# Optimization experiments

Hardware: AMD Instinct MI355X
Metric: run time of the kernel (lower is better)

The kernel has to match this reference:

```python
import jax, jax.numpy as jnp
import numpy as np

DIM = 1024
HEADS = 16
DH = DIM // HEADS
RANK = 4
B, S = 4, 1024
SCALE = 1.0 / np.sqrt(DH)
LN_EPS = 1e-5


def layer_norm(x, g, b):
    mu = jnp.mean(x, axis=-1, keepdims=True)
    var = jnp.mean((x - mu) ** 2, axis=-1, keepdims=True)
    return (x - mu) * jax.lax.rsqrt(var + LN_EPS) * g + b


def setup_inputs() -> dict:
    key = jax.random.key(0)
    ks = jax.random.split(key, 12)
    xav = lambda k, o, i: jax.random.uniform(k, (o, i), jnp.float32, -1.0, 1.0) * np.sqrt(6.0 / (o + i))
    return {
        "x": jax.random.normal(ks[0], (B, S, DIM), jnp.float32),
        "sigma": jnp.float32(0.1),
        "U": jax.random.normal(ks[1], (DIM, RANK), jnp.float32),
        "V": jax.random.normal(ks[2], (RANK, DIM), jnp.float32),
        "W_proj1": xav(ks[3], DIM, DIM // 2),
        "b_proj1": jnp.zeros((DIM,), jnp.float32),
        "W_proj2": xav(ks[4], DIM, DIM // 2),
        "b_proj2": jnp.zeros((DIM,), jnp.float32),
        "W_qkv1": xav(ks[5], 3 * DIM, DIM),
        "W_qkv2": xav(ks[6], 3 * DIM, DIM),
        "W_out": xav(ks[7], DIM, DIM),
        "b_out": jnp.zeros((DIM,), jnp.float32),
        "ln_g": jnp.ones((DIM,), jnp.float32),
        "ln_b": jnp.zeros((DIM,), jnp.float32),
    }


def _heads(t):  # [B,S,D] -> [B,H,S,dh]
    return t.reshape(B, S, HEADS, DH).transpose(0, 2, 1, 3)


def reference(x, sigma, U, V, W_proj1, b_proj1, W_proj2, b_proj2,
              W_qkv1, W_qkv2, W_out, b_out, ln_g, ln_b):
    # SVD adaptation bias: sigma*(U@V) summed over last dim -> [D], broadcast add
    svd_adapt = jnp.sum(sigma * (U @ V), axis=-1)  # [D]
    adapted_x = x + svd_adapt  # broadcast over [B,S,D]

    x1, x2 = jnp.split(adapted_x, 2, axis=-1)  # each [B,S,D/2]
    x1 = x1 @ W_proj1.T + b_proj1  # [B,S,D]
    x2 = x2 @ W_proj2.T + b_proj2

    q1, k1, v1 = jnp.split(x1 @ W_qkv1.T, 3, axis=-1)
    q2, k2, v2 = jnp.split(x2 @ W_qkv2.T, 3, axis=-1)
    q1, k1, v1 = _heads(q1), _heads(k1), _heads(v1)
    q2, k2, v2 = _heads(q2), _heads(k2), _heads(v2)

    # differential attention: softmax(q1k1) - softmax(q2k2), applied to (v1+v2)/2
    attn1 = jax.nn.softmax(jnp.einsum("bhqd,bhkd->bhqk", q1, k1) * SCALE, axis=-1)
    attn2 = jax.nn.softmax(jnp.einsum("bhqd,bhkd->bhqk", q2, k2) * SCALE, axis=-1)
    diff = attn1 - attn2
    out = jnp.einsum("bhqk,bhkd->bhqd", diff, (v1 + v2) * 0.5)

    out = out.transpose(0, 2, 1, 3).reshape(B, S, DIM)
    out = out @ W_out.T + b_out
    return layer_norm(out, ln_g, ln_b)
```

## Files before the change

### kernel.cpp

```cpp
#include <hip/hip_runtime.h>
#include <hip/hip_bf16.h>
#include <math.h>

#define DIMN   1024
#define HEADS  16
#define DHEAD  64
#define BQKV   3072
#define BATCH  4
#define SEQ    1024
#define NROWS  (BATCH * SEQ)
#define ATT_SCALE 0.125f
#define LN_EPS 1e-5f

typedef __attribute__((ext_vector_type(8))) short  bf16x8;
typedef __attribute__((ext_vector_type(4))) float  f32x4;
typedef __attribute__((ext_vector_type(4))) unsigned short u16x4;

__device__ __forceinline__ unsigned short f2bf(float f) {
    unsigned u = __float_as_uint(f);
    u += 0x7FFFu + ((u >> 16) & 1u);
    return (unsigned short)(u >> 16);
}
__device__ __forceinline__ float bf2f(unsigned short h) {
    return __uint_as_float((unsigned)h << 16);
}
__device__ __forceinline__ void gload_lds16(const void* g, void* l) {
    __builtin_amdgcn_global_load_lds(
        (const __attribute__((address_space(1))) unsigned int*)g,
        (__attribute__((address_space(3))) unsigned int*)l, 16, 0, 0);
}

__global__ __launch_bounds__(1024) void svd_kernel(
    const float* __restrict__ U, const float* __restrict__ V,
    const float* __restrict__ sigma_p, float* __restrict__ svd)
{
    __shared__ float part[16][4];
    __shared__ float vsum[4];
    const int tid = threadIdx.x;
    float v0 = V[0 * DIMN + tid];
    float v1 = V[1 * DIMN + tid];
    float v2 = V[2 * DIMN + tid];
    float v3 = V[3 * DIMN + tid];
    #pragma unroll
    for (int off = 32; off > 0; off >>= 1) {
        v0 += __shfl_down(v0, off);
        v1 += __shfl_down(v1, off);
        v2 += __shfl_down(v2, off);
        v3 += __shfl_down(v3, off);
    }
    const int lane = tid & 63, w = tid >> 6;
    if (lane == 0) { part[w][0] = v0; part[w][1] = v1; part[w][2] = v2; part[w][3] = v3; }
    __syncthreads();
    if (tid < 4) {
        float s = 0.f;
        #pragma unroll
        for (int i = 0; i < 16; ++i) s += part[i][tid];
        vsum[tid] = s;
    }
    __syncthreads();
    const float sg = sigma_p[0];
    float acc = U[tid * 4 + 0] * vsum[0] + U[tid * 4 + 1] * vsum[1]
              + U[tid * 4 + 2] * vsum[2] + U[tid * 4 + 3] * vsum[3];
    svd[tid] = sg * acc;
}

__global__ __launch_bounds__(256) void cvt_kernel(
    const float* __restrict__ src, unsigned short* __restrict__ dst)
{
    const int i = (blockIdx.x * 256 + threadIdx.x) * 8;
    float4 a = *(const float4*)(src + i);
    float4 b = *(const float4*)(src + i + 4);
    u16x4 h0, h1;
    h0[0] = f2bf(a.x); h0[1] = f2bf(a.y); h0[2] = f2bf(a.z); h0[3] = f2bf(a.w);
    h1[0] = f2bf(b.x); h1[1] = f2bf(b.y); h1[2] = f2bf(b.z); h1[3] = f2bf(b.w);
    *(u16x4*)(dst + i) = h0;
    *(u16x4*)(dst + i + 4) = h1;
}

__global__ __launch_bounds__(256) void xadapt_kernel(
    const float* __restrict__ x, const float* __restrict__ svd,
    unsigned short* __restrict__ out)
{
    const int i = (blockIdx.x * 256 + threadIdx.x) * 8;
    const int d = i & (DIMN - 1);
    float4 a = *(const float4*)(x + i);
    float4 b = *(const float4*)(x + i + 4);
    float4 sa = *(const float4*)(svd + d);
    float4 sb = *(const float4*)(svd + d + 4);
    u16x4 h0, h1;
    h0[0] = f2bf(a.x + sa.x); h0[1] = f2bf(a.y + sa.y);
    h0[2] = f2bf(a.z + sa.z); h0[3] = f2bf(a.w + sa.w);
    h1[0] = f2bf(b.x + sb.x); h1[1] = f2bf(b.y + sb.y);
    h1[2] = f2bf(b.z + sb.z); h1[3] = f2bf(b.w + sb.w);
    *(u16x4*)(out + i) = h0;
    *(u16x4*)(out + i + 4) = h1;
}

#define GBM 128
#define GBN 128
#define GBK 64

__global__ __launch_bounds__(256, 2) void gemm_bf16(
    const unsigned short* __restrict__ A, int lda,
    const unsigned short* __restrict__ W, int ldw,
    const float* __restrict__ bias,
    void* __restrict__ C, int ldc, int K, int out_bf16)
{
    __shared__ __align__(16) short As[GBM * GBK];
    __shared__ __align__(16) short Bs[GBN * GBK];
    const int tid = threadIdx.x;
    const int m0 = blockIdx.y * GBM;
    const int n0 = blockIdx.x * GBN;
    const int lane = tid & 63;
    const int wv = tid >> 6;
    const int wr = wv >> 1, wc = wv & 1;
    const int lr = lane & 15;
    const int kg = lane >> 4;

    f32x4 acc[4][4];
    #pragma unroll
    for (int i = 0; i < 4; ++i)
        #pragma unroll
        for (int j = 0; j < 4; ++j)
            acc[i][j] = (f32x4){0.f, 0.f, 0.f, 0.f};

    for (int k0 = 0; k0 < K; k0 += GBK) {
        #pragma unroll
        for (int i = 0; i < 4; ++i) {
            int flat = i * 256 + tid;
            int r = flat >> 3, c = flat & 7;
            int sc = c ^ (r & 7);
            gload_lds16(A + (size_t)(m0 + r) * lda + k0 + sc * 8, As + flat * 8);
        }
        #pragma unroll
        for (int i = 0; i < 4; ++i) {
            int flat = i * 256 + tid;
            int r = flat >> 3, c = flat & 7;
            int sc = c ^ (r & 7);
            gload_lds16(W + (size_t)(n0 + r) * ldw + k0 + sc * 8, Bs + flat * 8);
        }
        __syncthreads();

        #pragma unroll
        for (int ks = 0; ks < 2; ++ks) {
            bf16x8 a[4], b[4];
            #pragma unroll
            for (int mi = 0; mi < 4; ++mi) {
                int row = wr * 64 + mi * 16 + lr;
                int boff = row * 128 + (((ks * 4 + kg) ^ (row & 7)) << 4);
                a[mi] = *(const bf16x8*)((const char*)As + boff);
            }
            #pragma unroll
            for (int ni = 0; ni < 4; ++ni) {
                int row = wc * 64 + ni * 16 + lr;
                int boff = row * 128 + (((ks * 4 + kg) ^ (row & 7)) << 4);
                b[ni] = *(const bf16x8*)((const char*)Bs + boff);
            }
            #pragma unroll
            for (int mi = 0; mi < 4; ++mi)
                #pragma unroll
                for (int ni = 0; ni < 4; ++ni)
                    acc[mi][ni] = __builtin_amdgcn_mfma_f32_16x16x32_bf16(
                        a[mi], b[ni], acc[mi][ni], 0, 0, 0);
        }
        __syncthreads();
    }

    #pragma unroll
    for (int ni = 0; ni < 4; ++ni) {
        const int col = n0 + wc * 64 + ni * 16 + lr;
        const float bs = bias ? bias[col] : 0.f;
        #pragma unroll
        for (int mi = 0; mi < 4; ++mi) {
            const int row = m0 + wr * 64 + mi * 16 + kg * 4;
            #pragma unroll
            for (int r = 0; r < 4; ++r) {
                float v = acc[mi][ni][r] + bs;
                if (out_bf16)
                    ((unsigned short*)C)[(size_t)(row + r) * ldc + col] = f2bf(v);
                else
                    ((float*)C)[(size_t)(row + r) * ldc + col] = v;
            }
        }
    }
}

__global__ __launch_bounds__(256, 2) void attn_mfma(
    const unsigned short* __restrict__ qkv1,
    const unsigned short* __restrict__ qkv2,
    unsigned short* __restrict__ out)
{
    __shared__ __align__(16) short k1s[64 * 64];
    __shared__ __align__(16) short k2s[64 * 64];
    __shared__ __align__(16) short vts[64 * 64];
    __shared__ __align__(16) short pbufs[4][16 * 64];

    const int tid = threadIdx.x;
    const int lane = tid & 63;
    const int wv = tid >> 6;
    const int lr = lane & 15;
    const int kg = lane >> 4;
    const int bh = blockIdx.y;
    const int b = bh >> 4, h = bh & 15;
    const int bS = b * SEQ;
    const int q0w = blockIdx.x * 64 + wv * 16;
    short* pw = pbufs[wv];

    bf16x8 qf1[2], qf2[2];
    {
        const size_t qrow = (size_t)(bS + q0w + lr) * BQKV + h * DHEAD;
        #pragma unroll
        for (int ks = 0; ks < 2; ++ks) {
            const unsigned short* p1 = qkv1 + qrow + ks * 32 + kg * 8;
            const unsigned short* p2 = qkv2 + qrow + ks * 32 + kg * 8;
            bf16x8 f;
            #pragma unroll
            for (int j = 0; j < 8; ++j) f[j] = (short)f2bf(bf2f(p1[j]) * ATT_SCALE);
            qf1[ks] = f;
            #pragma unroll
            for (int j = 0; j < 8; ++j) f[j] = (short)f2bf(bf2f(p2[j]) * ATT_SCALE);
            qf2[ks] = f;
        }
    }

    f32x4 o1[4], o2[4];
    #pragma unroll
    for (int i = 0; i < 4; ++i) {
        o1[i] = (f32x4){0.f, 0.f, 0.f, 0.f};
        o2[i] = (f32x4){0.f, 0.f, 0.f, 0.f};
    }
    float m1 = -1e30f, l1 = 0.f, m2 = -1e30f, l2 = 0.f;

    for (int kt = 0; kt < SEQ; kt += 64) {
        #pragma unroll
        for (int i = 0; i < 2; ++i) {
            int flat = i * 256 + tid;
            int r = flat >> 3, c = flat & 7;
            int sc = c ^ (r & 7);
            size_t g = (size_t)(bS + kt + r) * BQKV + 1024 + h * DHEAD + sc * 8;
            gload_lds16(qkv1 + g, k1s + flat * 8);
            gload_lds16(qkv2 + g, k2s + flat * 8);
        }
        #pragma unroll
        for (int i = 0; i < 2; ++i) {
            int idx = i * 256 + tid;
            int kp = idx & 31;
            int dg = idx >> 5;
            size_t g = (size_t)(bS + kt + 2 * kp) * BQKV + 2048 + h * DHEAD + dg * 4;
            u16x4 x0 = *(const u16x4*)(qkv1 + g);
            u16x4 y0 = *(const u16x4*)(qkv2 + g);
            u16x4 x1 = *(const u16x4*)(qkv1 + g + BQKV);
            u16x4 y1 = *(const u16x4*)(qkv2 + g + BQKV);
            #pragma unroll
            for (int j = 0; j < 4; ++j) {
                float a = 0.5f * (bf2f(x0[j]) + bf2f(y0[j]));
                float c = 0.5f * (bf2f(x1[j]) + bf2f(y1[j]));
                unsigned pk = (unsigned)f2bf(a) | ((unsigned)f2bf(c) << 16);
                int dim = dg * 4 + j;
                int boff = dim * 128 + ((((kp >> 2) ^ (dim & 7)) << 4) | ((kp & 3) << 2));
                *(unsigned*)((char*)vts + boff) = pk;
            }
        }
        __syncthreads();

        f32x4 s1[4], s2[4];
        #pragma unroll
        for (int f = 0; f < 4; ++f) {
            s1[f] = (f32x4){0.f, 0.f, 0.f, 0.f};
            s2[f] = (f32x4){0.f, 0.f, 0.f, 0.f};
        }
        #pragma unroll
        for (int ks = 0; ks < 2; ++ks) {
            #pragma unroll
            for (int f = 0; f < 4; ++f) {
                int row = f * 16 + lr;
                int boff = row * 128 + (((ks * 4 + kg) ^ (row & 7)) << 4);
                bf16x8 a1 = *(const bf16x8*)((const char*)k1s + boff);
                bf16x8 a2 = *(const bf16x8*)((const char*)k2s + boff);
                s1[f] = __builtin_amdgcn_mfma_f32_16x16x32_bf16(a1, qf1[ks], s1[f], 0, 0, 0);
                s2[f] = __builtin_amdgcn_mfma_f32_16x16x32_bf16(a2, qf2[ks], s2[f], 0, 0, 0);
            }
        }

        #pragma unroll
        for (int br = 0; br < 2; ++br) {
            f32x4* sf = br ? s2 : s1;
            float& m = br ? m2 : m1;
            float& l = br ? l2 : l1;
            f32x4* oacc = br ? o2 : o1;

            float tm = -1e30f;
            #pragma unroll
            for (int f = 0; f < 4; ++f)
                #pragma unroll
                for (int r = 0; r < 4; ++r) tm = fmaxf(tm, sf[f][r]);
            tm = fmaxf(tm, __shfl_xor(tm, 16));
            tm = fmaxf(tm, __shfl_xor(tm, 32));
            float mnew = fmaxf(m, tm);
            float sc = __expf(m - mnew);
            m = mnew;

            float psum = 0.f;
            #pragma unroll
            for (int f = 0; f < 4; ++f) {
                u16x4 hw;
                #pragma unroll
                for (int r = 0; r < 4; ++r) {
                    float p = __expf(sf[f][r] - mnew);
                    unsigned short hb = f2bf(p);
                    hw[r] = hb;
                    psum += bf2f(hb);
                }
                int boff = lr * 128 + ((((f * 2 + (kg >> 1)) ^ (lr & 7)) << 4) | ((kg & 1) << 3));
                *(u16x4*)((char*)pw + boff) = hw;
            }
            psum += __shfl_xor(psum, 16);
            psum += __shfl_xor(psum, 32);
            l = l * sc + psum;

            #pragma unroll
            for (int r = 0; r < 4; ++r) {
                float scr = __shfl(sc, (kg << 2) | r);
                #pragma unroll
                for (int nf = 0; nf < 4; ++nf) oacc[nf][r] *= scr;
            }

            #pragma unroll
            for (int ks = 0; ks < 2; ++ks) {
                int boffp = lr * 128 + (((ks * 4 + kg) ^ (lr & 7)) << 4);
                bf16x8 ap = *(const bf16x8*)((const char*)pw + boffp);
                #pragma unroll
                for (int nf = 0; nf < 4; ++nf) {
                    int dim = nf * 16 + lr;
                    int boffv = dim * 128 + (((ks * 4 + kg) ^ (dim & 7)) << 4);
                    bf16x8 bv = *(const bf16x8*)((const char*)vts + boffv);
                    oacc[nf] = __builtin_amdgcn_mfma_f32_16x16x32_bf16(ap, bv, oacc[nf], 0, 0, 0);
                }
            }
        }
        __syncthreads();
    }

    const float inv1 = 1.f / l1, inv2 = 1.f / l2;
    #pragma unroll
    for (int r = 0; r < 4; ++r) {
        float r1 = __shfl(inv1, (kg << 2) | r);
        float r2 = __shfl(inv2, (kg << 2) | r);
        unsigned short* op = out + (size_t)(bS + q0w + kg * 4 + r) * DIMN + h * DHEAD + lr;
        #pragma unroll
        for (int nf = 0; nf < 4; ++nf)
            op[nf * 16] = f2bf(o1[nf][r] * r1 - o2[nf][r] * r2);
    }
}

__global__ __launch_bounds__(256) void ln_kernel(
    const float* __restrict__ X, const float* __restrict__ g,
    const float* __restrict__ bi, float* __restrict__ out)
{
    __shared__ float red[8];
    const int row = blockIdx.x;
    const int tid = threadIdx.x;
    const float* xp = X + (size_t)row * DIMN;
    float4 xv = *(const float4*)(xp + tid * 4);
    float s = xv.x + xv.y + xv.z + xv.w;
    #pragma unroll
    for (int off = 32; off > 0; off >>= 1) s += __shfl_down(s, off);
    const int lane = tid & 63, w = tid >> 6;
    if (lane == 0) red[w] = s;
    __syncthreads();
    const float mu = (red[0] + red[1] + red[2] + red[3]) * (1.f / DIMN);
    const float d0 = xv.x - mu, d1 = xv.y - mu, d2 = xv.z - mu, d3 = xv.w - mu;
    float sq = d0 * d0 + d1 * d1 + d2 * d2 + d3 * d3;
    #pragma unroll
    for (int off = 32; off > 0; off >>= 1) sq += __shfl_down(sq, off);
    if (lane == 0) red[4 + w] = sq;
    __syncthreads();
    const float var = (red[4] + red[5] + red[6] + red[7]) * (1.f / DIMN);
    const float inv = rsqrtf(var + LN_EPS);
    float4 gv = *(const float4*)(g + tid * 4);
    float4 bv = *(const float4*)(bi + tid * 4);
    float4 ov;
    ov.x = d0 * inv * gv.x + bv.x;
    ov.y = d1 * inv * gv.y + bv.y;
    ov.z = d2 * inv * gv.z + bv.z;
    ov.w = d3 * inv * gv.w + bv.w;
    *(float4*)(out + (size_t)row * DIMN + tid * 4) = ov;
}

extern "C" void kernel_launch(void* const* d_in, const int* in_sizes, int n_in,
                              void* d_out, int out_size, void* d_ws, size_t ws_size,
                              hipStream_t stream)
{
    const float* x     = (const float*)d_in[0];
    const float* sigma = (const float*)d_in[1];
    const float* U     = (const float*)d_in[2];
    const float* V     = (const float*)d_in[3];
    const float* Wp1   = (const float*)d_in[4];
    const float* bp1   = (const float*)d_in[5];
    const float* Wp2   = (const float*)d_in[6];
    const float* bp2   = (const float*)d_in[7];
    const float* Wqkv1 = (const float*)d_in[8];
    const float* Wqkv2 = (const float*)d_in[9];
    const float* Wout  = (const float*)d_in[10];
    const float* bout  = (const float*)d_in[11];
    const float* lng   = (const float*)d_in[12];
    const float* lnb   = (const float*)d_in[13];

    const size_t MB = 1024 * 1024;
    char* ws = (char*)d_ws;
    float*          svd    = (float*)(ws);
    unsigned short* wp1b   = (unsigned short*)(ws + 4096);
    unsigned short* wp2b   = (unsigned short*)(ws + 4096 + 1 * MB);
    unsigned short* wq1b   = (unsigned short*)(ws + 4096 + 2 * MB);
    unsigned short* wq2b   = (unsigned short*)(ws + 4096 + 8 * MB);
    unsigned short* woutb  = (unsigned short*)(ws + 4096 + 14 * MB);
    unsigned short* xadapt = (unsigned short*)(ws + 4096 + 16 * MB);
    unsigned short* x1p    = (unsigned short*)(ws + 4096 + 24 * MB);
    unsigned short* x2p    = (unsigned short*)(ws + 4096 + 32 * MB);
    unsigned short* qkv1b  = (unsigned short*)(ws + 4096 + 40 * MB);
    unsigned short* qkv2b  = (unsigned short*)(ws + 4096 + 64 * MB);
    unsigned short* attno  = (unsigned short*)(ws + 4096 + 88 * MB);
    float*          bufO   = (float*)(ws + 4096 + 96 * MB);

    svd_kernel<<<1, 1024, 0, stream>>>(U, V, sigma, svd);

    cvt_kernel<<<256,  256, 0, stream>>>(Wp1,   wp1b);
    cvt_kernel<<<256,  256, 0, stream>>>(Wp2,   wp2b);
    cvt_kernel<<<1536, 256, 0, stream>>>(Wqkv1, wq1b);
    cvt_kernel<<<1536, 256, 0, stream>>>(Wqkv2, wq2b);
    cvt_kernel<<<512,  256, 0, stream>>>(Wout,  woutb);
    xadapt_kernel<<<2048, 256, 0, stream>>>(x, svd, xadapt);

    gemm_bf16<<<dim3(DIMN / GBN, NROWS / GBM), 256, 0, stream>>>(
        xadapt, DIMN, wp1b, DIMN / 2, bp1, x1p, DIMN, DIMN / 2, 1);
    gemm_bf16<<<dim3(DIMN / GBN, NROWS / GBM), 256, 0, stream>>>(
        xadapt + DIMN / 2, DIMN, wp2b, DIMN / 2, bp2, x2p, DIMN, DIMN / 2, 1);
    gemm_bf16<<<dim3(BQKV / GBN, NROWS / GBM), 256, 0, stream>>>(
        x1p, DIMN, wq1b, DIMN, nullptr, qkv1b, BQKV, DIMN, 1);
    gemm_bf16<<<dim3(BQKV / GBN, NROWS / GBM), 256, 0, stream>>>(
        x2p, DIMN, wq2b, DIMN, nullptr, qkv2b, BQKV, DIMN, 1);

    attn_mfma<<<dim3(SEQ / 64, BATCH * HEADS), 256, 0, stream>>>(qkv1b, qkv2b, attno);

    gemm_bf16<<<dim3(DIMN / GBN, NROWS / GBM), 256, 0, stream>>>(
        attno, DIMN, woutb, DIMN, bout, bufO, DIMN, DIMN, 0);

    ln_kernel<<<NROWS, 256, 0, stream>>>(bufO, lng, lnb, (float*)d_out);
}
```

Before: 367.9 us.

## Fold projection weights into QKV weights and prefetch K/V tiles in attention

```diff
diff --git a/kernel.cpp b/kernel.cpp
--- a/kernel.cpp
+++ b/kernel.cpp
@@ -96,9 +96,211 @@
     *(u16x4*)(out + i + 4) = h1;
 }
 
-#define GBM 128
-#define GBN 128
-#define GBK 64
+__global__ __launch_bounds__(256, 2) void wprep_kernel(
+    const float* __restrict__ Wq1, const float* __restrict__ Wp1,
+    const float* __restrict__ Wq2, const float* __restrict__ Wp2,
+    unsigned short* __restrict__ Wt1, unsigned short* __restrict__ Wt2)
+{
+    const float* Wq = blockIdx.z ? Wq2 : Wq1;
+    const float* Wp = blockIdx.z ? Wp2 : Wp1;
+    unsigned short* Wt = blockIdx.z ? Wt2 : Wt1;
+
+    __shared__ __align__(16) short As[128 * 64];
+    __shared__ __align__(16) short Bs[128 * 64];
+    const int tid = threadIdx.x;
+    const int m0 = blockIdx.y * 128;
+    const int n0 = blockIdx.x * 128;
+    const int lane = tid & 63;
+    const int wv = tid >> 6;
+    const int wr = wv >> 1, wc = wv & 1;
+    const int lr = lane & 15;
+    const int kg = lane >> 4;
+
+    f32x4 acc[4][4];
+    #pragma unroll
+    for (int i = 0; i < 4; ++i)
+        #pragma unroll
+        for (int j = 0; j < 4; ++j)
+            acc[i][j] = (f32x4){0.f, 0.f, 0.f, 0.f};
+
+    for (int k0 = 0; k0 < DIMN; k0 += 64) {
+        #pragma unroll
+        for (int i = 0; i < 8; ++i) {
+            int flat = i * 256 + tid;
+            int r  = flat >> 4;
+            int c4 = flat & 15;
+            float4 av = *(const float4*)(Wq + (size_t)(m0 + r) * DIMN + k0 + c4 * 4);
+            u16x4 h;
+            h[0] = f2bf(av.x); h[1] = f2bf(av.y); h[2] = f2bf(av.z); h[3] = f2bf(av.w);
+            int boff = r * 128 + ((((c4 >> 1) ^ (r & 7)) << 4) | ((c4 & 1) << 3));
+            *(u16x4*)((char*)As + boff) = h;
+        }
+        #pragma unroll
+        for (int i = 0; i < 4; ++i) {
+            int idx = i * 256 + tid;
+            int kp = idx & 31;
+            int dg = idx >> 5;
+            const float* p0 = Wp + (size_t)(k0 + 2 * kp) * 512 + n0 + dg * 4;
+            float4 x0 = *(const float4*)p0;
+            float4 x1 = *(const float4*)(p0 + 512);
+            float a0[4] = {x0.x, x0.y, x0.z, x0.w};
+            float a1[4] = {x1.x, x1.y, x1.z, x1.w};
+            #pragma unroll
+            for (int j = 0; j < 4; ++j) {
+                unsigned pk = (unsigned)f2bf(a0[j]) | ((unsigned)f2bf(a1[j]) << 16);
+                int n = dg * 4 + j;
+                int boff = n * 128 + ((((kp >> 2) ^ (n & 7)) << 4) | ((kp & 3) << 2));
+                *(unsigned*)((char*)Bs + boff) = pk;
+            }
+        }
+        __syncthreads();
+
+        #pragma unroll
+        for (int ks = 0; ks < 2; ++ks) {
+            bf16x8 a[4], b[4];
+            #pragma unroll
+            for (int mi = 0; mi < 4; ++mi) {
+                int row = wr * 64 + mi * 16 + lr;
+                int boff = row * 128 + (((ks * 4 + kg) ^ (row & 7)) << 4);
+                a[mi] = *(const bf16x8*)((const char*)As + boff);
+            }
+            #pragma unroll
+            for (int ni = 0; ni < 4; ++ni) {
+                int row = wc * 64 + ni * 16 + lr;
+                int boff = row * 128 + (((ks * 4 + kg) ^ (row & 7)) << 4);
+                b[ni] = *(const bf16x8*)((const char*)Bs + boff);
+            }
+            #pragma unroll
+            for (int mi = 0; mi < 4; ++mi)
+                #pragma unroll
+                for (int ni = 0; ni < 4; ++ni)
+                    acc[mi][ni] = __builtin_amdgcn_mfma_f32_16x16x32_bf16(
+                        a[mi], b[ni], acc[mi][ni], 0, 0, 0);
+        }
+        __syncthreads();
+    }
+
+    #pragma unroll
+    for (int ni = 0; ni < 4; ++ni) {
+        const int col = n0 + wc * 64 + ni * 16 + lr;
+        #pragma unroll
+        for (int mi = 0; mi < 4; ++mi) {
+            const int row = m0 + wr * 64 + mi * 16 + kg * 4;
+            #pragma unroll
+            for (int r = 0; r < 4; ++r) {
+                float sc = (row + r) < DIMN ? ATT_SCALE : 1.f;
+                Wt[(size_t)(row + r) * 512 + col] = f2bf(acc[mi][ni][r] * sc);
+            }
+        }
+    }
+}
+
+__global__ __launch_bounds__(256) void bvec_kernel(
+    const float* __restrict__ Wq1, const float* __restrict__ bp1,
+    const float* __restrict__ Wq2, const float* __restrict__ bp2,
+    float* __restrict__ bt1, float* __restrict__ bt2)
+{
+    const float* Wq = blockIdx.y ? Wq2 : Wq1;
+    const float* bp = blockIdx.y ? bp2 : bp1;
+    float* bt = blockIdx.y ? bt2 : bt1;
+    const int i = blockIdx.x * 256 + threadIdx.x;
+    const float* row = Wq + (size_t)i * DIMN;
+    float s = 0.f;
+    for (int k = 0; k < DIMN; k += 4) {
+        float4 wv = *(const float4*)(row + k);
+        float4 bv = *(const float4*)(bp + k);
+        s += wv.x * bv.x + wv.y * bv.y + wv.z * bv.z + wv.w * bv.w;
+    }
+    bt[i] = (i < DIMN ? ATT_SCALE : 1.f) * s;
+}
+
+__global__ __launch_bounds__(256, 2) void gemm_qkv(
+    const unsigned short* __restrict__ xadapt,
+    const unsigned short* __restrict__ Wt1,
+    const unsigned short* __restrict__ Wt2,
+    const float* __restrict__ bt1,
+    const float* __restrict__ bt2,
+    unsigned short* __restrict__ C1,
+    unsigned short* __restrict__ C2)
+{
+    const unsigned short* A = xadapt + (blockIdx.z ? 512 : 0);
+    const unsigned short* W = blockIdx.z ? Wt2 : Wt1;
+    const float* bias = blockIdx.z ? bt2 : bt1;
+    unsigned short* C = blockIdx.z ? C2 : C1;
+
+    __shared__ __align__(16) short As[128 * 64];
+    __shared__ __align__(16) short Bs[128 * 64];
+    const int tid = threadIdx.x;
+    const int m0 = blockIdx.y * 128;
+    const int n0 = blockIdx.x * 128;
+    const int lane = tid & 63;
+    const int wv = tid >> 6;
+    const int wr = wv >> 1, wc = wv & 1;
+    const int lr = lane & 15;
+    const int kg = lane >> 4;
+
+    f32x4 acc[4][4];
+    #pragma unroll
+    for (int i = 0; i < 4; ++i)
+        #pragma unroll
+        for (int j = 0; j < 4; ++j)
+            acc[i][j] = (f32x4){0.f, 0.f, 0.f, 0.f};
+
+    for (int k0 = 0; k0 < 512; k0 += 64) {
+        #pragma unroll
+        for (int i = 0; i < 4; ++i) {
+            int flat = i * 256 + tid;
+            int r = flat >> 3, c = flat & 7;
+            int sc = c ^ (r & 7);
+            gload_lds16(A + (size_t)(m0 + r) * DIMN + k0 + sc * 8, As + flat * 8);
+        }
+        #pragma unroll
+        for (int i = 0; i < 4; ++i) {
+            int flat = i * 256 + tid;
+            int r = flat >> 3, c = flat & 7;
+            int sc = c ^ (r & 7);
+            gload_lds16(W + (size_t)(n0 + r) * 512 + k0 + sc * 8, Bs + flat * 8);
+        }
+        __syncthreads();
+
+        #pragma unroll
+        for (int ks = 0; ks < 2; ++ks) {
+            bf16x8 a[4], b[4];
+            #pragma unroll
+            for (int mi = 0; mi < 4; ++mi) {
+                int row = wr * 64 + mi * 16 + lr;
+                int boff = row * 128 + (((ks * 4 + kg) ^ (row & 7)) << 4);
+                a[mi] = *(const bf16x8*)((const char*)As + boff);
+            }
+            #pragma unroll
+            for (int ni = 0; ni < 4; ++ni) {
+                int row = wc * 64 + ni * 16 + lr;
+                int boff = row * 128 + (((ks * 4 + kg) ^ (row & 7)) << 4);
+                b[ni] = *(const bf16x8*)((const char*)Bs + boff);
+            }
+            #pragma unroll
+            for (int mi = 0; mi < 4; ++mi)
+                #pragma unroll
+                for (int ni = 0; ni < 4; ++ni)
+                    acc[mi][ni] = __builtin_amdgcn_mfma_f32_16x16x32_bf16(
+                        a[mi], b[ni], acc[mi][ni], 0, 0, 0);
+        }
+        __syncthreads();
+    }
+
+    #pragma unroll
+    for (int ni = 0; ni < 4; ++ni) {
+        const int col = n0 + wc * 64 + ni * 16 + lr;
+        const float bs = bias[col];
+        #pragma unroll
+        for (int mi = 0; mi < 4; ++mi) {
+            const int row = m0 + wr * 64 + mi * 16 + kg * 4;
+            #pragma unroll
+            for (int r = 0; r < 4; ++r)
+                C[(size_t)(row + r) * BQKV + col] = f2bf(acc[mi][ni][r] + bs);
+        }
+    }
+}
 
 __global__ __launch_bounds__(256, 2) void gemm_bf16(
     const unsigned short* __restrict__ A, int lda,
@@ -106,11 +308,11 @@
     const float* __restrict__ bias,
     void* __restrict__ C, int ldc, int K, int out_bf16)
 {
-    __shared__ __align__(16) short As[GBM * GBK];
-    __shared__ __align__(16) short Bs[GBN * GBK];
+    __shared__ __align__(16) short As[128 * 64];
+    __shared__ __align__(16) short Bs[128 * 64];
     const int tid = threadIdx.x;
-    const int m0 = blockIdx.y * GBM;
-    const int n0 = blockIdx.x * GBN;
+    const int m0 = blockIdx.y * 128;
+    const int n0 = blockIdx.x * 128;
     const int lane = tid & 63;
     const int wv = tid >> 6;
     const int wr = wv >> 1, wc = wv & 1;
@@ -124,7 +326,7 @@
         for (int j = 0; j < 4; ++j)
             acc[i][j] = (f32x4){0.f, 0.f, 0.f, 0.f};
 
-    for (int k0 = 0; k0 < K; k0 += GBK) {
+    for (int k0 = 0; k0 < K; k0 += 64) {
         #pragma unroll
         for (int i = 0; i < 4; ++i) {
             int flat = i * 256 + tid;
@@ -185,7 +387,7 @@
     }
 }
 
-__global__ __launch_bounds__(256, 2) void attn_mfma(
+__global__ __launch_bounds__(256, 3) void attn_mfma(
     const unsigned short* __restrict__ qkv1,
     const unsigned short* __restrict__ qkv2,
     unsigned short* __restrict__ out)
@@ -206,62 +408,77 @@
     const int q0w = blockIdx.x * 64 + wv * 16;
     short* pw = pbufs[wv];
 
-    bf16x8 qf1[2], qf2[2];
-    {
-        const size_t qrow = (size_t)(bS + q0w + lr) * BQKV + h * DHEAD;
-        #pragma unroll
-        for (int ks = 0; ks < 2; ++ks) {
-            const unsigned short* p1 = qkv1 + qrow + ks * 32 + kg * 8;
-            const unsigned short* p2 = qkv2 + qrow + ks * 32 + kg * 8;
-            bf16x8 f;
-            #pragma unroll
-            for (int j = 0; j < 8; ++j) f[j] = (short)f2bf(bf2f(p1[j]) * ATT_SCALE);
-            qf1[ks] = f;
-            #pragma unroll
-            for (int j = 0; j < 8; ++j) f[j] = (short)f2bf(bf2f(p2[j]) * ATT_SCALE);
-            qf2[ks] = f;
-        }
-    }
-
-    f32x4 o1[4], o2[4];
-    #pragma unroll
-    for (int i = 0; i < 4; ++i) {
-        o1[i] = (f32x4){0.f, 0.f, 0.f, 0.f};
-        o2[i] = (f32x4){0.f, 0.f, 0.f, 0.f};
-    }
-    float m1 = -1e30f, l1 = 0.f, m2 = -1e30f, l2 = 0.f;
-
-    for (int kt = 0; kt < SEQ; kt += 64) {
-        #pragma unroll
-        for (int i = 0; i < 2; ++i) {
-            int flat = i * 256 + tid;
-            int r = flat >> 3, c = flat & 7;
-            int sc = c ^ (r & 7);
-            size_t g = (size_t)(bS + kt + r) * BQKV + 1024 + h * DHEAD + sc * 8;
-            gload_lds16(qkv1 + g, k1s + flat * 8);
-            gload_lds16(qkv2 + g, k2s + flat * 8);
-        }
+    bf16x8 rk1[2], rk2[2];
+    u16x4  rv[2][4];
+
+    const int krow = tid >> 2;
+    const int kc4  = tid & 3;
+
+    auto LOADT = [&](int kt) {
+        size_t g = (size_t)(bS + kt + krow) * BQKV + 1024 + h * DHEAD + kc4 * 16;
+        rk1[0] = *(const bf16x8*)(qkv1 + g);
+        rk1[1] = *(const bf16x8*)(qkv1 + g + 8);
+        rk2[0] = *(const bf16x8*)(qkv2 + g);
+        rk2[1] = *(const bf16x8*)(qkv2 + g + 8);
         #pragma unroll
         for (int i = 0; i < 2; ++i) {
             int idx = i * 256 + tid;
-            int kp = idx & 31;
-            int dg = idx >> 5;
-            size_t g = (size_t)(bS + kt + 2 * kp) * BQKV + 2048 + h * DHEAD + dg * 4;
-            u16x4 x0 = *(const u16x4*)(qkv1 + g);
-            u16x4 y0 = *(const u16x4*)(qkv2 + g);
-            u16x4 x1 = *(const u16x4*)(qkv1 + g + BQKV);
-            u16x4 y1 = *(const u16x4*)(qkv2 + g + BQKV);
+            int kp = idx & 31, dg = idx >> 5;
+            size_t gv = (size_t)(bS + kt + 2 * kp) * BQKV + 2048 + h * DHEAD + dg * 4;
+            rv[i][0] = *(const u16x4*)(qkv1 + gv);
+            rv[i][1] = *(const u16x4*)(qkv2 + gv);
+            rv[i][2] = *(const u16x4*)(qkv1 + gv + BQKV);
+            rv[i][3] = *(const u16x4*)(qkv2 + gv + BQKV);
+        }
+    };
+    auto WRITET = [&]() {
+        int b0 = krow * 128 + (((kc4 * 2) ^ (krow & 7)) << 4);
+        int b1 = krow * 128 + (((kc4 * 2 + 1) ^ (krow & 7)) << 4);
+        *(bf16x8*)((char*)k1s + b0) = rk1[0];
+        *(bf16x8*)((char*)k1s + b1) = rk1[1];
+        *(bf16x8*)((char*)k2s + b0) = rk2[0];
+        *(bf16x8*)((char*)k2s + b1) = rk2[1];
+        #pragma unroll
+        for (int i = 0; i < 2; ++i) {
+            int idx = i * 256 + tid;
+            int kp = idx & 31, dg = idx >> 5;
             #pragma unroll
             for (int j = 0; j < 4; ++j) {
-                float a = 0.5f * (bf2f(x0[j]) + bf2f(y0[j]));
-                float c = 0.5f * (bf2f(x1[j]) + bf2f(y1[j]));
+                float a = 0.5f * (bf2f(rv[i][0][j]) + bf2f(rv[i][1][j]));
+                float c = 0.5f * (bf2f(rv[i][2][j]) + bf2f(rv[i][3][j]));
                 unsigned pk = (unsigned)f2bf(a) | ((unsigned)f2bf(c) << 16);
                 int dim = dg * 4 + j;
                 int boff = dim * 128 + ((((kp >> 2) ^ (dim & 7)) << 4) | ((kp & 3) << 2));
                 *(unsigned*)((char*)vts + boff) = pk;
             }
         }
-        __syncthreads();
+    };
+
+    bf16x8 qf1[2], qf2[2];
+    {
+        const size_t qrow = (size_t)(bS + q0w + lr) * BQKV + h * DHEAD;
+        #pragma unroll
+        for (int ks = 0; ks < 2; ++ks) {
+            qf1[ks] = *(const bf16x8*)(qkv1 + qrow + ks * 32 + kg * 8);
+            qf2[ks] = *(const bf16x8*)(qkv2 + qrow + ks * 32 + kg * 8);
+        }
+    }
+
+    f32x4 o1[4], o2[4];
+    #pragma unroll
+    for (int i = 0; i < 4; ++i) {
+        o1[i] = (f32x4){0.f, 0.f, 0.f, 0.f};
+        o2[i] = (f32x4){0.f, 0.f, 0.f, 0.f};
+    }
+    float m1 = -1e30f, l1 = 0.f, m2 = -1e30f, l2 = 0.f;
+
+    LOADT(0);
+    WRITET();
+    __syncthreads();
+
+    for (int kt = 0; kt < SEQ; kt += 64) {
+        const bool more = (kt + 64) < SEQ;
+        if (more) LOADT(kt + 64);
 
         f32x4 s1[4], s2[4];
         #pragma unroll
@@ -307,9 +524,8 @@
                 #pragma unroll
                 for (int r = 0; r < 4; ++r) {
                     float p = __expf(sf[f][r] - mnew);
-                    unsigned short hb = f2bf(p);
-                    hw[r] = hb;
-                    psum += bf2f(hb);
+                    hw[r] = f2bf(p);
+                    psum += p;
                 }
                 int boff = lr * 128 + ((((f * 2 + (kg >> 1)) ^ (lr & 7)) << 4) | ((kg & 1) << 3));
                 *(u16x4*)((char*)pw + boff) = hw;
@@ -338,7 +554,12 @@
                 }
             }
         }
+
         __syncthreads();
+        if (more) {
+            WRITET();
+            __syncthreads();
+        }
     }
 
     const float inv1 = 1.f / l1, inv2 = 1.f / l2;
@@ -409,40 +630,30 @@
     const size_t MB = 1024 * 1024;
     char* ws = (char*)d_ws;
     float*          svd    = (float*)(ws);
-    unsigned short* wp1b   = (unsigned short*)(ws + 4096);
-    unsigned short* wp2b   = (unsigned short*)(ws + 4096 + 1 * MB);
-    unsigned short* wq1b   = (unsigned short*)(ws + 4096 + 2 * MB);
-    unsigned short* wq2b   = (unsigned short*)(ws + 4096 + 8 * MB);
-    unsigned short* woutb  = (unsigned short*)(ws + 4096 + 14 * MB);
-    unsigned short* xadapt = (unsigned short*)(ws + 4096 + 16 * MB);
-    unsigned short* x1p    = (unsigned short*)(ws + 4096 + 24 * MB);
-    unsigned short* x2p    = (unsigned short*)(ws + 4096 + 32 * MB);
-    unsigned short* qkv1b  = (unsigned short*)(ws + 4096 + 40 * MB);
-    unsigned short* qkv2b  = (unsigned short*)(ws + 4096 + 64 * MB);
-    unsigned short* attno  = (unsigned short*)(ws + 4096 + 88 * MB);
-    float*          bufO   = (float*)(ws + 4096 + 96 * MB);
+    float*          bt1    = (float*)(ws + 4096);
+    float*          bt2    = (float*)(ws + 16384);
+    unsigned short* woutb  = (unsigned short*)(ws + 1 * MB);
+    unsigned short* wt1    = (unsigned short*)(ws + 3 * MB);
+    unsigned short* wt2    = (unsigned short*)(ws + 6 * MB);
+    unsigned short* xadapt = (unsigned short*)(ws + 9 * MB);
+    unsigned short* qkv1b  = (unsigned short*)(ws + 17 * MB);
+    unsigned short* qkv2b  = (unsigned short*)(ws + 41 * MB);
+    unsigned short* attno  = (unsigned short*)(ws + 65 * MB);
+    float*          bufO   = (float*)(ws + 73 * MB);
 
     svd_kernel<<<1, 1024, 0, stream>>>(U, V, sigma, svd);
-
-    cvt_kernel<<<256,  256, 0, stream>>>(Wp1,   wp1b);
-    cvt_kernel<<<256,  256, 0, stream>>>(Wp2,   wp2b);
-    cvt_kernel<<<1536, 256, 0, stream>>>(Wqkv1, wq1b);
-    cvt_kernel<<<1536, 256, 0, stream>>>(Wqkv2, wq2b);
-    cvt_kernel<<<512,  256, 0, stream>>>(Wout,  woutb);
     xadapt_kernel<<<2048, 256, 0, stream>>>(x, svd, xadapt);
 
-    gemm_bf16<<<dim3(DIMN / GBN, NROWS / GBM), 256, 0, stream>>>(
-        xadapt, DIMN, wp1b, DIMN / 2, bp1, x1p, DIMN, DIMN / 2, 1);
-    gemm_bf16<<<dim3(DIMN / GBN, NROWS / GBM), 256, 0, stream>>>(
-        xadapt + DIMN / 2, DIMN, wp2b, DIMN / 2, bp2, x2p, DIMN, DIMN / 2, 1);
-    gemm_bf16<<<dim3(BQKV / GBN, NROWS / GBM), 256, 0, stream>>>(
-        x1p, DIMN, wq1b, DIMN, nullptr, qkv1b, BQKV, DIMN, 1);
-    gemm_bf16<<<dim3(BQKV / GBN, NROWS / GBM), 256, 0, stream>>>(
-        x2p, DIMN, wq2b, DIMN, nullptr, qkv2b, BQKV, DIMN, 1);
+    wprep_kernel<<<dim3(4, 24, 2), 256, 0, stream>>>(Wqkv1, Wp1, Wqkv2, Wp2, wt1, wt2);
+    bvec_kernel<<<dim3(12, 2), 256, 0, stream>>>(Wqkv1, bp1, Wqkv2, bp2, bt1, bt2);
+    cvt_kernel<<<512, 256, 0, stream>>>(Wout, woutb);
+
+    gemm_qkv<<<dim3(BQKV / 128, NROWS / 128, 2), 256, 0, stream>>>(
+        xadapt, wt1, wt2, bt1, bt2, qkv1b, qkv2b);
 
     attn_mfma<<<dim3(SEQ / 64, BATCH * HEADS), 256, 0, stream>>>(qkv1b, qkv2b, attno);
 
-    gemm_bf16<<<dim3(DIMN / GBN, NROWS / GBM), 256, 0, stream>>>(
+    gemm_bf16<<<dim3(DIMN / 128, NROWS / 128), 256, 0, stream>>>(
         attno, DIMN, woutb, DIMN, bout, bufO, DIMN, DIMN, 0);
 
     ln_kernel<<<NROWS, 256, 0, stream>>>(bufO, lng, lnb, (float*)d_out);
```

After: 400.4 us. 8.9% more time.
